# Kernel optimization log

Hardware: AMD Instinct MI355X
Metric: run time of the kernel (lower is better)

Reference implementation:

```python
import jax, jax.numpy as jnp
import numpy as np
from jax import lax

T, B, I, H = 32768, 1, 128, 512  # seq_len, batch(=1 due to squeeze(1)), input_dim, hidden_dim
HEAD = 25

def setup_inputs() -> dict:
    key = jax.random.key(0)
    ks = jax.random.split(key, 8)
    s = 1.0 / np.sqrt(H)  # pytorch LSTM init scale
    return {
        "x": jax.random.normal(ks[0], (T, B, I), dtype=jnp.float32),
        "W_ih": jax.random.uniform(ks[1], (4 * H, I), jnp.float32, -s, s),
        "W_hh": jax.random.uniform(ks[2], (4 * H, H), jnp.float32, -s, s),
        "b_ih": jax.random.uniform(ks[3], (4 * H,), jnp.float32, -s, s),
        "b_hh": jax.random.uniform(ks[4], (4 * H,), jnp.float32, -s, s),
        "W1": jax.random.uniform(ks[5], (HEAD, H), jnp.float32, -s, s),
        "b1": jax.random.uniform(ks[6], (HEAD,), jnp.float32, -s, s),
        "Wout": jax.random.uniform(ks[7], (1, HEAD), jnp.float32, -s, s),
    }

def reference(x, W_ih, W_hh, b_ih, b_hh, W1, b1, Wout):
    # Precompute input projections for all timesteps (one big GEMM): [T, B, 4H]
    xg = jnp.einsum('tbi,gi->tbg', x, W_ih) + (b_ih + b_hh)

    def step(carry, xg_t):
        h, c = carry  # [B, H] each
        gates = xg_t + h @ W_hh.T  # [B, 4H]
        i_g, f_g, g_g, o_g = jnp.split(gates, 4, axis=-1)  # pytorch gate order i,f,g,o
        i = jax.nn.sigmoid(i_g)
        f = jax.nn.sigmoid(f_g)
        g = jnp.tanh(g_g)
        o = jax.nn.sigmoid(o_g)
        c = f * c + i * g
        h = o * jnp.tanh(c)
        return (h, c), h

    h0 = jnp.zeros((B, H), x.dtype)
    _, hs = lax.scan(step, (h0, h0), xg)  # hs: [T, B, H]

    hid = hs[:, 0, :]  # h_1.squeeze(1) -> [T, H]
    # forward applies c1 then out (c2 is defined but unused in the original)
    out = (hid @ W1.T + b1) @ Wout.T  # [T, 1]
    return out
```

## Files before the change

### kernel.cpp

```cpp
#include <hip/hip_runtime.h>
#include <math.h>


#define T_SEQ 32768
#define HID   512
#define INP   128
#define NWG   32
#define NTH   512
#define HSL   16
#define KW    64
#define KX    16
#define NPK   256

typedef unsigned long long u64;
typedef unsigned int u32;

__device__ __forceinline__ float fast_sigmoid(float x) {
    return 1.0f / (1.0f + __expf(-x));
}
__device__ __forceinline__ float fast_tanh(float x) {
    float a = fabsf(x);
    float e = __expf(-2.0f * a);
    float r = (1.0f - e) / (1.0f + e);
    return copysignf(r, x);
}

__global__ void __launch_bounds__(NTH, 2) lstm_persist(
    const float* __restrict__ x,
    const float* __restrict__ W_ih,
    const float* __restrict__ W_hh,
    const float* __restrict__ b_ih,
    const float* __restrict__ b_hh,
    const float* __restrict__ W1,
    const float* __restrict__ b1,
    const float* __restrict__ Wout,
    u64* __restrict__ hbuf,
    float* __restrict__ out)
{
    const int w   = blockIdx.x;
    const int tid = threadIdx.x;
    const int wv  = tid >> 6;
    const int l   = tid & 63;
    const int rw  = l >> 3;
    const int j   = l & 7;
    const int g   = rw >> 1;
    const int b   = rw & 1;
    const bool is_out = (w == 0 && wv == 1);

    __shared__ float h_lds[2][HID];

    const int grow = g * HID + w * HSL + 2 * wv + b;

    float wr[KW], wi[KX];
#pragma unroll
    for (int kk = 0; kk < 16; ++kk) {
        const int p = (kk + 2 * j) & 15;
        const float4 v4 = *(const float4*)&W_hh[grow * HID + j * KW + 4 * p];
        wr[4 * kk + 0] = v4.x; wr[4 * kk + 1] = v4.y;
        wr[4 * kk + 2] = v4.z; wr[4 * kk + 3] = v4.w;
    }
#pragma unroll
    for (int k = 0; k < KX; k += 4) {
        const float4 v4 = *(const float4*)&W_ih[grow * INP + j * KX + k];
        wi[k] = v4.x; wi[k + 1] = v4.y; wi[k + 2] = v4.z; wi[k + 3] = v4.w;
    }
    float brow = b_ih[grow] + b_hh[grow];

    float weff_o[8];
    float be = 0.0f;
#pragma unroll
    for (int i = 0; i < 8; ++i) weff_o[i] = 0.0f;
    if (is_out) {
#pragma unroll
        for (int i = 0; i < 8; ++i) {
            float s = 0.0f;
            for (int p = 0; p < 25; ++p) s += Wout[p] * W1[p * HID + l + 64 * i];
            weff_o[i] = s;
        }
        for (int p = 0; p < 25; ++p) be += b1[p] * Wout[p];
    }
#pragma unroll
    for (int k = 0; k < KW; ++k) asm volatile("" : "+v"(wr[k]));
#pragma unroll
    for (int k = 0; k < KX; ++k) asm volatile("" : "+v"(wi[k]));
#pragma unroll
    for (int i = 0; i < 8; ++i) asm volatile("" : "+v"(weff_o[i]));
    asm volatile("" : "+v"(brow));
    asm volatile("" : "+v"(be));

    float c = 0.0f;
    float xa[KX];
#pragma unroll
    for (int k = 0; k < KX; ++k) xa[k] = x[j * KX + k];

    for (u32 t = 0; t <= T_SEQ; ++t) {
        if (t == T_SEQ && w != 0) break;

        if (wv == 0) {
            const u64* P = hbuf + (t & 1) * NPK;
            float2* HL = (float2*)h_lds[t & 1];
            bool mine = false;
            while (true) {
                if (!mine) {
                    u64 pr[4];
                    bool ok = true;
#pragma unroll
                    for (int i = 0; i < 4; ++i) {
                        pr[i] = __hip_atomic_load(&P[l + 64 * i],
                                                  __ATOMIC_RELAXED,
                                                  __HIP_MEMORY_SCOPE_AGENT);
                        ok = ok && ((((u32)pr[i]) ^ t) & 15u) == 0u;
                    }
                    if (ok) {
#pragma unroll
                        for (int i = 0; i < 4; ++i) {
                            float2 hp;
                            hp.x = __uint_as_float((u32)pr[i]);
                            hp.y = __uint_as_float((u32)(pr[i] >> 32));
                            HL[l + 64 * i] = hp;
                        }
                        mine = true;
                    }
                }
                if (__ballot(mine) == ~0ull) break;
            }
        }
        __syncthreads();

        float hv = 0.0f;
        if (t < T_SEQ) {
            float a0 = 0.0f, a1 = 0.0f, a2 = 0.0f, a3 = 0.0f;
#pragma unroll
            for (int k = 0; k < KX; k += 4) {
                a0 += wi[k + 0] * xa[k + 0];
                a1 += wi[k + 1] * xa[k + 1];
                a2 += wi[k + 2] * xa[k + 2];
                a3 += wi[k + 3] * xa[k + 3];
            }
            const float4* hl4 = (const float4*)&h_lds[t & 1][j * KW];
#pragma unroll
            for (int kk = 0; kk < 16; ++kk) {
                const int p = (kk + 2 * j) & 15;
                const float4 h4 = hl4[p];
                a0 += wr[4 * kk + 0] * h4.x;
                a1 += wr[4 * kk + 1] * h4.y;
                a2 += wr[4 * kk + 2] * h4.z;
                a3 += wr[4 * kk + 3] * h4.w;
            }
            const int tn = (t + 1 < T_SEQ) ? (int)(t + 1) : (T_SEQ - 1);
#pragma unroll
            for (int k = 0; k < KX; k += 4) {
                const float4 x4 = *(const float4*)&x[tn * INP + j * KX + k];
                xa[k + 0] = x4.x; xa[k + 1] = x4.y;
                xa[k + 2] = x4.z; xa[k + 3] = x4.w;
            }
            float acc = (a0 + a1) + (a2 + a3);
            acc += __shfl_xor(acc, 1);
            acc += __shfl_xor(acc, 2);
            acc += __shfl_xor(acc, 4);
            acc += brow;
            const float ig = acc;
            const float fg = __shfl(acc, l + 16);
            const float gg = __shfl(acc, l + 32);
            const float og = __shfl(acc, l + 48);
            const float iv = fast_sigmoid(ig);
            const float fv = fast_sigmoid(fg);
            const float gv = fast_tanh(gg);
            const float ov = fast_sigmoid(og);
            c = fv * c + iv * gv;
            hv = ov * fast_tanh(c);
            const float hv1 = __shfl(hv, 8);
            if (l == 0) {
                const u32 b0 = (__float_as_uint(hv) & ~15u) | ((t + 1) & 15u);
                const u32 b1v = __float_as_uint(hv1);
                const u64 pkt = ((u64)b1v << 32) | (u64)b0;
                __hip_atomic_store(&hbuf[((t + 1) & 1) * NPK + w * 8 + wv], pkt,
                                   __ATOMIC_RELAXED, __HIP_MEMORY_SCOPE_AGENT);
            }
        }

        if (is_out && t >= 1) {
            float pd = 0.0f;
#pragma unroll
            for (int i = 0; i < 8; ++i)
                pd += h_lds[t & 1][l + 64 * i] * weff_o[i];
            pd += __shfl_xor(pd, 1);
            pd += __shfl_xor(pd, 2);
            pd += __shfl_xor(pd, 4);
            pd += __shfl_xor(pd, 8);
            pd += __shfl_xor(pd, 16);
            pd += __shfl_xor(pd, 32);
            if (l == 0) out[t - 1] = pd + be;
        }
    }
}

extern "C" void kernel_launch(void* const* d_in, const int* in_sizes, int n_in,
                              void* d_out, int out_size, void* d_ws, size_t ws_size,
                              hipStream_t stream)
{
    const float* x    = (const float*)d_in[0];
    const float* W_ih = (const float*)d_in[1];
    const float* W_hh = (const float*)d_in[2];
    const float* b_ih = (const float*)d_in[3];
    const float* b_hh = (const float*)d_in[4];
    const float* W1   = (const float*)d_in[5];
    const float* b1   = (const float*)d_in[6];
    const float* Wout = (const float*)d_in[7];
    float* out = (float*)d_out;

    u64* hbuf = (u64*)d_ws;

    hipMemsetAsync(d_ws, 0, 2 * NPK * sizeof(u64), stream);
    lstm_persist<<<NWG, NTH, 0, stream>>>(x, W_ih, W_hh, b_ih, b_hh, W1, b1,
                                          Wout, hbuf, out);
}
```

Baseline: 65.79 ms.

## Have every wave poll the global h buffer directly, dropping LDS staging and block barriers

```diff
diff --git a/kernel.cpp b/kernel.cpp
--- a/kernel.cpp
+++ b/kernel.cpp
@@ -7,9 +7,6 @@
 #define INP   128
 #define NWG   32
 #define NTH   512
-#define HSL   16
-#define KW    64
-#define KX    16
 #define NPK   256
 
 typedef unsigned long long u64;
@@ -25,7 +22,7 @@
     return copysignf(r, x);
 }
 
-__global__ void __launch_bounds__(NTH, 2) lstm_persist(
+__global__ void __launch_bounds__(NTH, 1) lstm_persist(
     const float* __restrict__ x,
     const float* __restrict__ W_ih,
     const float* __restrict__ W_hh,
@@ -41,31 +38,31 @@
     const int tid = threadIdx.x;
     const int wv  = tid >> 6;
     const int l   = tid & 63;
-    const int rw  = l >> 3;
-    const int j   = l & 7;
-    const int g   = rw >> 1;
-    const int b   = rw & 1;
+    const int odd = l & 1;
     const bool is_out = (w == 0 && wv == 1);
 
-    __shared__ float h_lds[2][HID];
-
-    const int grow = g * HID + w * HSL + 2 * wv + b;
-
-    float wr[KW], wi[KX];
-#pragma unroll
-    for (int kk = 0; kk < 16; ++kk) {
-        const int p = (kk + 2 * j) & 15;
-        const float4 v4 = *(const float4*)&W_hh[grow * HID + j * KW + 4 * p];
-        wr[4 * kk + 0] = v4.x; wr[4 * kk + 1] = v4.y;
-        wr[4 * kk + 2] = v4.z; wr[4 * kk + 3] = v4.w;
-    }
-#pragma unroll
-    for (int k = 0; k < KX; k += 4) {
-        const float4 v4 = *(const float4*)&W_ih[grow * INP + j * KX + k];
-        wi[k] = v4.x; wi[k + 1] = v4.y; wi[k + 2] = v4.z; wi[k + 3] = v4.w;
-    }
-    float brow = b_ih[grow] + b_hh[grow];
-
+    const int e0 = w * 16 + 2 * wv;
+
+    float wr[8][8];
+    float wi0[8], wi1[8];
+#pragma unroll
+    for (int r = 0; r < 8; ++r) {
+        const int grow = (r >> 1) * HID + e0 + (r & 1);
+        const float4 a4 = *(const float4*)&W_hh[grow * HID + 8 * l];
+        const float4 b4 = *(const float4*)&W_hh[grow * HID + 8 * l + 4];
+        wr[r][0] = a4.x; wr[r][1] = a4.y; wr[r][2] = a4.z; wr[r][3] = a4.w;
+        wr[r][4] = b4.x; wr[r][5] = b4.y; wr[r][6] = b4.z; wr[r][7] = b4.w;
+        const float2 x2 = *(const float2*)&W_ih[grow * INP + 2 * l];
+        wi0[r] = x2.x; wi1[r] = x2.y;
+    }
+    float bI, bF, bG, bO;
+    {
+        const int e = e0 + odd;
+        bI = b_ih[0 * HID + e] + b_hh[0 * HID + e];
+        bF = b_ih[1 * HID + e] + b_hh[1 * HID + e];
+        bG = b_ih[2 * HID + e] + b_hh[2 * HID + e];
+        bO = b_ih[3 * HID + e] + b_hh[3 * HID + e];
+    }
     float weff_o[8];
     float be = 0.0f;
 #pragma unroll
@@ -74,122 +71,108 @@
 #pragma unroll
         for (int i = 0; i < 8; ++i) {
             float s = 0.0f;
-            for (int p = 0; p < 25; ++p) s += Wout[p] * W1[p * HID + l + 64 * i];
+            for (int p = 0; p < 25; ++p) s += Wout[p] * W1[p * HID + 8 * l + i];
             weff_o[i] = s;
         }
         for (int p = 0; p < 25; ++p) be += b1[p] * Wout[p];
     }
 #pragma unroll
-    for (int k = 0; k < KW; ++k) asm volatile("" : "+v"(wr[k]));
-#pragma unroll
-    for (int k = 0; k < KX; ++k) asm volatile("" : "+v"(wi[k]));
-#pragma unroll
-    for (int i = 0; i < 8; ++i) asm volatile("" : "+v"(weff_o[i]));
-    asm volatile("" : "+v"(brow));
+    for (int r = 0; r < 8; ++r) {
+#pragma unroll
+        for (int k = 0; k < 8; ++k) asm volatile("" : "+v"(wr[r][k]));
+        asm volatile("" : "+v"(wi0[r]));
+        asm volatile("" : "+v"(wi1[r]));
+        asm volatile("" : "+v"(weff_o[r]));
+    }
+    asm volatile("" : "+v"(bI)); asm volatile("" : "+v"(bF));
+    asm volatile("" : "+v"(bG)); asm volatile("" : "+v"(bO));
     asm volatile("" : "+v"(be));
 
     float c = 0.0f;
-    float xa[KX];
-#pragma unroll
-    for (int k = 0; k < KX; ++k) xa[k] = x[j * KX + k];
+    float2 xv = *(const float2*)&x[2 * l];
+    float x0 = xv.x, x1 = xv.y;
+
+    bool dead = false;
 
     for (u32 t = 0; t <= T_SEQ; ++t) {
-        if (t == T_SEQ && w != 0) break;
-
-        if (wv == 0) {
-            const u64* P = hbuf + (t & 1) * NPK;
-            float2* HL = (float2*)h_lds[t & 1];
+        if (t == T_SEQ && !is_out) break;
+
+        float acc[8];
+#pragma unroll
+        for (int r = 0; r < 8; ++r) acc[r] = wi0[r] * x0 + wi1[r] * x1;
+        const int tn = (t + 1 < T_SEQ) ? (int)(t + 1) : (T_SEQ - 1);
+        {
+            const float2 nv = *(const float2*)&x[tn * INP + 2 * l];
+            x0 = nv.x; x1 = nv.y;
+        }
+
+        u64 pr[4] = {0, 0, 0, 0};
+        if (!dead) {
+            const u64* P = hbuf + (t & 1) * NPK + 4 * l;
             bool mine = false;
+            int guard = 0;
             while (true) {
                 if (!mine) {
-                    u64 pr[4];
                     bool ok = true;
 #pragma unroll
                     for (int i = 0; i < 4; ++i) {
-                        pr[i] = __hip_atomic_load(&P[l + 64 * i],
-                                                  __ATOMIC_RELAXED,
+                        pr[i] = __hip_atomic_load(&P[i], __ATOMIC_RELAXED,
                                                   __HIP_MEMORY_SCOPE_AGENT);
                         ok = ok && ((((u32)pr[i]) ^ t) & 15u) == 0u;
                     }
-                    if (ok) {
-#pragma unroll
-                        for (int i = 0; i < 4; ++i) {
-                            float2 hp;
-                            hp.x = __uint_as_float((u32)pr[i]);
-                            hp.y = __uint_as_float((u32)(pr[i] >> 32));
-                            HL[l + 64 * i] = hp;
-                        }
-                        mine = true;
-                    }
+                    mine = ok;
                 }
                 if (__ballot(mine) == ~0ull) break;
-            }
-        }
-        __syncthreads();
-
-        float hv = 0.0f;
+                if (++guard > (1 << 22)) { dead = true; break; }
+            }
+        }
+
         if (t < T_SEQ) {
-            float a0 = 0.0f, a1 = 0.0f, a2 = 0.0f, a3 = 0.0f;
-#pragma unroll
-            for (int k = 0; k < KX; k += 4) {
-                a0 += wi[k + 0] * xa[k + 0];
-                a1 += wi[k + 1] * xa[k + 1];
-                a2 += wi[k + 2] * xa[k + 2];
-                a3 += wi[k + 3] * xa[k + 3];
-            }
-            const float4* hl4 = (const float4*)&h_lds[t & 1][j * KW];
-#pragma unroll
-            for (int kk = 0; kk < 16; ++kk) {
-                const int p = (kk + 2 * j) & 15;
-                const float4 h4 = hl4[p];
-                a0 += wr[4 * kk + 0] * h4.x;
-                a1 += wr[4 * kk + 1] * h4.y;
-                a2 += wr[4 * kk + 2] * h4.z;
-                a3 += wr[4 * kk + 3] * h4.w;
-            }
-            const int tn = (t + 1 < T_SEQ) ? (int)(t + 1) : (T_SEQ - 1);
-#pragma unroll
-            for (int k = 0; k < KX; k += 4) {
-                const float4 x4 = *(const float4*)&x[tn * INP + j * KX + k];
-                xa[k + 0] = x4.x; xa[k + 1] = x4.y;
-                xa[k + 2] = x4.z; xa[k + 3] = x4.w;
-            }
-            float acc = (a0 + a1) + (a2 + a3);
-            acc += __shfl_xor(acc, 1);
-            acc += __shfl_xor(acc, 2);
-            acc += __shfl_xor(acc, 4);
-            acc += brow;
-            const float ig = acc;
-            const float fg = __shfl(acc, l + 16);
-            const float gg = __shfl(acc, l + 32);
-            const float og = __shfl(acc, l + 48);
-            const float iv = fast_sigmoid(ig);
-            const float fv = fast_sigmoid(fg);
-            const float gv = fast_tanh(gg);
-            const float ov = fast_sigmoid(og);
+#pragma unroll
+            for (int i = 0; i < 4; ++i) {
+                const float hlo = __uint_as_float((u32)pr[i]);
+                const float hhi = __uint_as_float((u32)(pr[i] >> 32));
+#pragma unroll
+                for (int r = 0; r < 8; ++r)
+                    acc[r] += wr[r][2 * i] * hlo + wr[r][2 * i + 1] * hhi;
+            }
+#pragma unroll
+            for (int s = 1; s < 64; s <<= 1) {
+#pragma unroll
+                for (int r = 0; r < 8; ++r)
+                    acc[r] += __shfl_xor(acc[r], s);
+            }
+            const float gI = (odd ? acc[1] : acc[0]) + bI;
+            const float gF = (odd ? acc[3] : acc[2]) + bF;
+            const float gG = (odd ? acc[5] : acc[4]) + bG;
+            const float gO = (odd ? acc[7] : acc[6]) + bO;
+            const float iv = fast_sigmoid(gI);
+            const float fv = fast_sigmoid(gF);
+            const float gv = fast_tanh(gG);
+            const float ov = fast_sigmoid(gO);
             c = fv * c + iv * gv;
-            hv = ov * fast_tanh(c);
-            const float hv1 = __shfl(hv, 8);
+            const float hv = ov * fast_tanh(c);
+            const float h0 = __shfl(hv, 0);
+            const float h1 = __shfl(hv, 1);
             if (l == 0) {
-                const u32 b0 = (__float_as_uint(hv) & ~15u) | ((t + 1) & 15u);
-                const u32 b1v = __float_as_uint(hv1);
-                const u64 pkt = ((u64)b1v << 32) | (u64)b0;
-                __hip_atomic_store(&hbuf[((t + 1) & 1) * NPK + w * 8 + wv], pkt,
-                                   __ATOMIC_RELAXED, __HIP_MEMORY_SCOPE_AGENT);
+                const u32 b0 = (__float_as_uint(h0) & ~15u) | ((t + 1) & 15u);
+                const u64 pkt = ((u64)__float_as_uint(h1) << 32) | (u64)b0;
+                (void)__hip_atomic_exchange(
+                    &hbuf[((t + 1) & 1) * NPK + w * 8 + wv], pkt,
+                    __ATOMIC_RELAXED, __HIP_MEMORY_SCOPE_AGENT);
             }
         }
 
         if (is_out && t >= 1) {
             float pd = 0.0f;
 #pragma unroll
-            for (int i = 0; i < 8; ++i)
-                pd += h_lds[t & 1][l + 64 * i] * weff_o[i];
-            pd += __shfl_xor(pd, 1);
-            pd += __shfl_xor(pd, 2);
-            pd += __shfl_xor(pd, 4);
-            pd += __shfl_xor(pd, 8);
-            pd += __shfl_xor(pd, 16);
-            pd += __shfl_xor(pd, 32);
+            for (int i = 0; i < 4; ++i) {
+                pd += weff_o[2 * i]     * __uint_as_float((u32)pr[i]);
+                pd += weff_o[2 * i + 1] * __uint_as_float((u32)(pr[i] >> 32));
+            }
+#pragma unroll
+            for (int s = 1; s < 64; s <<= 1)
+                pd += __shfl_xor(pd, s);
             if (l == 0) out[t - 1] = pd + be;
         }
     }
```

Result: slower. 127.6 ms (+93.9%).
